# Performance work log

Measured on AMD Instinct MI355X. Metric: run time of the kernel, lower is better.

The kernel has to match this reference:

```python
import jax, jax.numpy as jnp
import numpy as np

N_NODES = 100000
N_EDGES = 1600000
IN_CH = 128
TYPE_EMB = 32
OUT_CH = 128
N_REL = 8
N_BASES = 8
N_NTYPES = 8
FEAT = IN_CH + TYPE_EMB  # 160, RGCNConv input dim after concat


def setup_inputs() -> dict:
    key = jax.random.key(0)
    ks = jax.random.split(key, 9)
    x = jax.random.normal(ks[0], (N_NODES, IN_CH), dtype=jnp.float32)
    node_type_ids = jax.random.randint(ks[1], (N_NODES,), 0, N_NTYPES)
    edge_index = jax.random.randint(ks[2], (2, N_EDGES), 0, N_NODES)
    edge_type = jax.random.randint(ks[3], (N_EDGES,), 0, N_REL)
    emb_table = jax.random.normal(ks[4], (N_NTYPES, TYPE_EMB), dtype=jnp.float32)
    bases = jax.random.normal(ks[5], (N_BASES, FEAT, OUT_CH), dtype=jnp.float32) * (1.0 / np.sqrt(FEAT))
    comp = jax.random.normal(ks[6], (N_REL, N_BASES), dtype=jnp.float32) * (1.0 / np.sqrt(N_BASES))
    root_w = jax.random.normal(ks[7], (FEAT, OUT_CH), dtype=jnp.float32) * (1.0 / np.sqrt(FEAT))
    bias = jnp.zeros((OUT_CH,), dtype=jnp.float32)
    return {"x": x, "node_type_ids": node_type_ids, "edge_index": edge_index,
            "edge_type": edge_type, "emb_table": emb_table, "bases": bases,
            "comp": comp, "root_w": root_w, "bias": bias}


def reference(x, node_type_ids, edge_index, edge_type, emb_table, bases, comp, root_w, bias):
    N = x.shape[0]
    # node-type embedding lookup + concat
    h = jnp.concatenate([x, emb_table[node_type_ids]], axis=1)  # [N, FEAT]
    # basis decomposition: per-relation weights [R, FEAT, OUT]
    weight = jnp.einsum('rb,bio->rio', comp, bases)
    src, dst = edge_index[0], edge_index[1]
    h_src = h[src]  # [E, FEAT] -- dominant gather
    # root/self transform + bias
    out = h @ root_w + bias
    # PyG RGCNConv default aggr='mean': per-relation mean over incoming edges, summed across relations
    for r in range(weight.shape[0]):
        m = (edge_type == r).astype(h.dtype)  # [E]
        s = jax.ops.segment_sum(h_src * m[:, None], dst, num_segments=N)  # [N, FEAT]
        c = jax.ops.segment_sum(m, dst, num_segments=N)                    # [N]
        mean_r = s / jnp.maximum(c, 1.0)[:, None]
        out = out + mean_r @ weight[r]
    # dropout is identity in eval mode
    return jax.nn.relu(out)
```

## Files before the change

### kernel.cpp

```cpp
#include <hip/hip_runtime.h>

#define NN 100000
#define NE 1600000
#define INC 128
#define TE 32
#define OC 128
#define NR 8
#define NBASES 8
#define FT 160
#define KP 168
#define KW 160
#define TN 64
#define NBKT 1563
#define NCH 512
#define EPB 3125
#define CAP 1536

typedef float f32x4 __attribute__((ext_vector_type(4)));
typedef __bf16 bf16x8 __attribute__((ext_vector_type(8)));

__device__ __forceinline__ unsigned f2bf1(float f) {
    unsigned u = __float_as_uint(f);
    return (u + 0x7fffu + ((u >> 16) & 1u)) >> 16;
}

__device__ __forceinline__ int bscan_excl(int v, int* tmp) {
    int tid = threadIdx.x;
    tmp[tid] = v; __syncthreads();
#pragma unroll
    for (int d = 1; d < 256; d <<= 1) {
        int t = (tid >= d) ? tmp[tid - d] : 0;
        __syncthreads();
        tmp[tid] += t;
        __syncthreads();
    }
    return tmp[tid] - v;
}

__global__ void k_prep(const float* __restrict__ x, const int* __restrict__ nt,
                       const float* __restrict__ emb, const float* __restrict__ comp,
                       const float* __restrict__ bases, const float* __restrict__ rootw,
                       unsigned short* __restrict__ h, unsigned short* __restrict__ Wt) {
    int idx = blockIdx.x * 256 + threadIdx.x;
    if (idx < 9 * 128 * KW) {
        int ridx = idx / (128 * KW);
        int rem  = idx % (128 * KW);
        int o = rem / KW;
        int k = rem % KW;
        float v;
        if (ridx < NR) {
            v = 0.f;
#pragma unroll
            for (int b = 0; b < NBASES; b++)
                v += comp[ridx * NBASES + b] * bases[(b * FT + k) * OC + o];
        } else {
            v = rootw[k * OC + o];
        }
        Wt[idx] = (unsigned short)f2bf1(v);
    }
    if (idx < NN * 20) {
        int n = idx / 20, c = idx % 20;
        f32x4 v0, v1;
        if (c < 16) {
            const float* p = x + (size_t)n * INC + c * 8;
            v0 = *(const f32x4*)p; v1 = *(const f32x4*)(p + 4);
        } else {
            int tt = nt[n];
            const float* p = emb + tt * TE + (c - 16) * 8;
            v0 = *(const f32x4*)p; v1 = *(const f32x4*)(p + 4);
        }
        uint4 o;
        o.x = f2bf1(v0.x) | (f2bf1(v0.y) << 16);
        o.y = f2bf1(v0.z) | (f2bf1(v0.w) << 16);
        o.z = f2bf1(v1.x) | (f2bf1(v1.y) << 16);
        o.w = f2bf1(v1.z) | (f2bf1(v1.w) << 16);
        *(uint4*)(h + (size_t)n * FT + c * 8) = o;
    }
}

__global__ __launch_bounds__(256) void k_hist(const int* __restrict__ ei, int* __restrict__ ghist) {
    __shared__ int hist[NBKT];
    int tid = threadIdx.x;
    for (int j = tid; j < NBKT; j += 256) hist[j] = 0;
    __syncthreads();
    int e0 = blockIdx.x * EPB;
#pragma unroll
    for (int k = 0; k < 13; k++) {
        int i = k * 256 + tid;
        if (i < EPB) atomicAdd(&hist[ei[NE + e0 + i] >> 6], 1);
    }
    __syncthreads();
    int* g = ghist + (size_t)blockIdx.x * NBKT;
    for (int j = tid; j < NBKT; j += 256) g[j] = hist[j];
}

__global__ void k_total(const int* __restrict__ ghist, int* __restrict__ total) {
    int j = blockIdx.x * 256 + threadIdx.x;
    if (j >= NBKT) return;
    int s = 0;
#pragma unroll 8
    for (int b = 0; b < NCH; b++) s += ghist[(size_t)b * NBKT + j];
    total[j] = s;
}

__global__ void k_scanTot(const int* __restrict__ total, int* __restrict__ bstart) {
    __shared__ int tmp[256];
    int tid = threadIdx.x, s = 0, i0 = tid * 7;
#pragma unroll
    for (int i = 0; i < 7; i++) { int j = i0 + i; if (j < NBKT) s += total[j]; }
    int run = bscan_excl(s, tmp);
#pragma unroll
    for (int i = 0; i < 7; i++) { int j = i0 + i; if (j < NBKT) { bstart[j] = run; run += total[j]; } }
    if (tid == 0) bstart[NBKT] = NE;
}

__global__ void k_offsets(int* __restrict__ ghist, const int* __restrict__ bstart) {
    int j = blockIdx.x * 256 + threadIdx.x;
    if (j >= NBKT) return;
    int run = bstart[j];
#pragma unroll 4
    for (int b = 0; b < NCH; b++) {
        int v = ghist[(size_t)b * NBKT + j];
        ghist[(size_t)b * NBKT + j] = run;
        run += v;
    }
}

__global__ __launch_bounds__(256) void k_scatter(const int* __restrict__ ei, const int* __restrict__ et,
                                                 const int* __restrict__ ghist, unsigned* __restrict__ slots) {
    __shared__ int cur[NBKT];
    int tid = threadIdx.x, b = blockIdx.x;
    for (int j = tid; j < NBKT; j += 256) cur[j] = ghist[(size_t)b * NBKT + j];
    __syncthreads();
    int e0 = b * EPB;
#pragma unroll
    for (int k = 0; k < 13; k++) {
        int i = k * 256 + tid;
        if (i < EPB) {
            int e = e0 + i;
            int s = ei[e], d = ei[NE + e], r = et[e];
            int pos = atomicAdd(&cur[d >> 6], 1);
            slots[pos] = (unsigned)s | ((unsigned)r << 17) | ((unsigned)(d & 63) << 20);
        }
    }
}

__global__ __launch_bounds__(256, 5) void k_mega(
    const unsigned short* __restrict__ h, const float* __restrict__ bias,
    const unsigned short* __restrict__ Wt, const int* __restrict__ bstart,
    const unsigned* __restrict__ slots, float* __restrict__ out) {
    __shared__ unsigned short featmem[TN * KP];
    __shared__ unsigned sl[CAP];
    __shared__ unsigned pkl[512];

    const int tid = threadIdx.x;
    const int lane = tid & 63;
    const int wave = tid >> 6;
    const int j = blockIdx.x;
    const int n0 = j * TN;

    unsigned* sl_in = reinterpret_cast<unsigned*>(featmem);
    int* hist = reinterpret_cast<int*>(featmem) + CAP;
    int* tmp  = reinterpret_cast<int*>(featmem) + CAP + 512;

    int s0 = bstart[j];
    int m = bstart[j + 1] - s0; if (m > CAP) m = CAP;
    for (int i = tid; i < m; i += 256) sl_in[i] = slots[s0 + i];
    for (int k = tid; k < 512; k += 256) hist[k] = 0;
    __syncthreads();
    for (int i = tid; i < m; i += 256) {
        unsigned v = sl_in[i];
        atomicAdd(&hist[((v >> 17) & 7u) * 64u + ((v >> 20) & 63u)], 1);
    }
    __syncthreads();
    int v0 = hist[2 * tid], v1 = hist[2 * tid + 1];
    int ex = bscan_excl(v0 + v1, tmp);
    pkl[2 * tid]     = (unsigned)ex | ((unsigned)v0 << 16);
    pkl[2 * tid + 1] = (unsigned)(ex + v0) | ((unsigned)v1 << 16);
    hist[2 * tid] = ex; hist[2 * tid + 1] = ex + v0;
    __syncthreads();
    for (int i = tid; i < m; i += 256) {
        unsigned v = sl_in[i];
        int p = atomicAdd(&hist[((v >> 17) & 7u) * 64u + ((v >> 20) & 63u)], 1);
        sl[p] = v & 0x03F1FFFFu;
    }
    __syncthreads();

    for (int i = tid; i < TN * 20; i += 256) {
        int nl = i / 20, c = i % 20, n = n0 + nl;
        uint4 v = (uint4){0u, 0u, 0u, 0u};
        if (n < NN) v = *reinterpret_cast<const uint4*>(h + (size_t)n * FT + c * 8);
        *reinterpret_cast<uint4*>(&featmem[nl * KP + c * 8]) = v;
    }

    f32x4 acc[8];
#pragma unroll
    for (int t = 0; t < 8; t++) acc[t] = (f32x4){0.f, 0.f, 0.f, 0.f};

    auto mfma_pass = [&](int ridx) {
        const unsigned short* fA = featmem + (lane & 15) * KP + ((lane >> 4) * 8);
        const unsigned short* gB = Wt + (size_t)ridx * 128 * KW
                                   + (wave * 32 + (lane & 15)) * KW + ((lane >> 4) * 8);
#pragma unroll
        for (int kc = 0; kc < 5; kc++) {
            bf16x8 a0 = *reinterpret_cast<const bf16x8*>(fA + 0 * 16 * KP + kc * 32);
            bf16x8 a1 = *reinterpret_cast<const bf16x8*>(fA + 1 * 16 * KP + kc * 32);
            bf16x8 a2 = *reinterpret_cast<const bf16x8*>(fA + 2 * 16 * KP + kc * 32);
            bf16x8 a3 = *reinterpret_cast<const bf16x8*>(fA + 3 * 16 * KP + kc * 32);
#pragma unroll
            for (int ct = 0; ct < 2; ct++) {
                bf16x8 b = *reinterpret_cast<const bf16x8*>(gB + ct * 16 * KW + kc * 32);
                acc[0 * 2 + ct] = __builtin_amdgcn_mfma_f32_16x16x32_bf16(a0, b, acc[0 * 2 + ct], 0, 0, 0);
                acc[1 * 2 + ct] = __builtin_amdgcn_mfma_f32_16x16x32_bf16(a1, b, acc[1 * 2 + ct], 0, 0, 0);
                acc[2 * 2 + ct] = __builtin_amdgcn_mfma_f32_16x16x32_bf16(a2, b, acc[2 * 2 + ct], 0, 0, 0);
                acc[3 * 2 + ct] = __builtin_amdgcn_mfma_f32_16x16x32_bf16(a3, b, acc[3 * 2 + ct], 0, 0, 0);
            }
        }
    };

    __syncthreads();
    mfma_pass(8);

    const int g = tid >> 4, l = tid & 15;
    const unsigned* hw = reinterpret_cast<const unsigned*>(h);
    for (int r = 0; r < NR; r++) {
        __syncthreads();
        int b0 = r * 64 + 4 * g;
        unsigned pa = pkl[b0], pd = pkl[b0 + 3];
        int sbeg = (int)(pa & 0xffffu);
        int send = (int)(pd & 0xffffu) + (int)(pd >> 16);
        float sa[10];
#pragma unroll
        for (int i = 0; i < 10; i++) sa[i] = 0.f;
        float run = 0.f;
        unsigned cur5[5]; int curdl = 0;
        if (sbeg < send) {
            unsigned v = sl[sbeg];
            const unsigned* hp = hw + (size_t)(v & 0x1FFFFu) * 80 + l;
#pragma unroll
            for (int c = 0; c < 5; c++) cur5[c] = hp[c * 16];
            curdl = (int)((v >> 20) & 63u);
        }
        for (int e = sbeg; e < send; e++) {
            int en = (e + 1 < send) ? e + 1 : e;
            unsigned vn = sl[en];
            const unsigned* hp = hw + (size_t)(vn & 0x1FFFFu) * 80 + l;
            unsigned nx[5];
#pragma unroll
            for (int c = 0; c < 5; c++) nx[c] = hp[c * 16];
            int nxdl = (int)((vn >> 20) & 63u);
#pragma unroll
            for (int c = 0; c < 5; c++) {
                sa[2 * c]     += __uint_as_float(cur5[c] << 16);
                sa[2 * c + 1] += __uint_as_float(cur5[c] & 0xFFFF0000u);
            }
            run += 1.f;
            bool fl = (e + 1 >= send) || (nxdl != curdl);
            if (fl) {
                float inv = 1.0f / run;
                unsigned* fp = reinterpret_cast<unsigned*>(featmem + curdl * KP) + l;
#pragma unroll
                for (int c = 0; c < 5; c++)
                    fp[c * 16] = f2bf1(sa[2 * c] * inv) | (f2bf1(sa[2 * c + 1] * inv) << 16);
#pragma unroll
                for (int i = 0; i < 10; i++) sa[i] = 0.f;
                run = 0.f;
            }
#pragma unroll
            for (int c = 0; c < 5; c++) cur5[c] = nx[c];
            curdl = nxdl;
        }
#pragma unroll
        for (int q = 0; q < 4; q++) {
            if ((pkl[b0 + q] >> 16) == 0u) {
                unsigned* fp = reinterpret_cast<unsigned*>(featmem + (4 * g + q) * KP) + l;
#pragma unroll
                for (int c = 0; c < 5; c++) fp[c * 16] = 0u;
            }
        }
        __syncthreads();
        mfma_pass(r);
    }

    const int rq = lane >> 4;
#pragma unroll
    for (int ct = 0; ct < 2; ct++) {
        int col = wave * 32 + ct * 16 + (lane & 15);
        float bv = bias[col];
#pragma unroll
        for (int rt = 0; rt < 4; rt++) {
#pragma unroll
            for (int i = 0; i < 4; i++) {
                int n = n0 + rt * 16 + rq * 4 + i;
                if (n < NN) {
                    float v = acc[rt * 2 + ct][i] + bv;
                    out[(size_t)n * OC + col] = v > 0.f ? v : 0.f;
                }
            }
        }
    }
}

extern "C" void kernel_launch(void* const* d_in, const int* in_sizes, int n_in,
                              void* d_out, int out_size, void* d_ws, size_t ws_size,
                              hipStream_t stream) {
    const float* x     = (const float*)d_in[0];
    const int*   ntype = (const int*)d_in[1];
    const int*   ei    = (const int*)d_in[2];
    const int*   et    = (const int*)d_in[3];
    const float* emb   = (const float*)d_in[4];
    const float* bases = (const float*)d_in[5];
    const float* comp  = (const float*)d_in[6];
    const float* rootw = (const float*)d_in[7];
    const float* bias  = (const float*)d_in[8];
    float* out = (float*)d_out;

    char* ws = (char*)d_ws;
    unsigned short* Wt     = (unsigned short*)(ws);
    unsigned short* h      = (unsigned short*)(ws + 368640);
    int*            ghist  = (int*)(ws + 32368640);
    int*            total  = (int*)(ws + 35569664);
    int*            bstart = (int*)(ws + 35576064);
    unsigned*       slots  = (unsigned*)(ws + 35582464);

    k_prep   <<<7813, 256, 0, stream>>>(x, ntype, emb, comp, bases, rootw, h, Wt);
    k_hist   <<<NCH,  256, 0, stream>>>(ei, ghist);
    k_total  <<<7,    256, 0, stream>>>(ghist, total);
    k_scanTot<<<1,    256, 0, stream>>>(total, bstart);
    k_offsets<<<7,    256, 0, stream>>>(ghist, bstart);
    k_scatter<<<NCH,  256, 0, stream>>>(ei, et, ghist, slots);
    k_mega   <<<NBKT, 256, 0, stream>>>(h, bias, Wt, bstart, slots, out);
}
```

Baseline: 372.4 us.

## Fuse histogram into prep kernel, coarsen edge chunks, unroll gather loop

Folds the edge histogram into the prep kernel as extra blocks, which removes one launch. The edge chunk count drops from 512 to 128, shrinking the per-chunk histogram arrays and the offset scan work that loops over chunks. The mega kernel's gather loop now issues four edges' row loads at once instead of one-ahead software pipelining, and its occupancy hint is relaxed from 5 to 4 blocks. Trade-offs: fewer, longer histogram and scatter blocks lower parallelism, and the unrolled gather raises register pressure.

Measured after the change: 353.2 us. -5.2%, faster.

```diff
diff --git a/kernel.cpp b/kernel.cpp
--- a/kernel.cpp
+++ b/kernel.cpp
@@ -12,8 +12,8 @@
 #define KW 160
 #define TN 64
 #define NBKT 1563
-#define NCH 512
-#define EPB 3125
+#define NCH 128
+#define EPB 12500
 #define CAP 1536
 
 typedef float f32x4 __attribute__((ext_vector_type(4)));
@@ -37,11 +37,31 @@
     return tmp[tid] - v;
 }
 
-__global__ void k_prep(const float* __restrict__ x, const int* __restrict__ nt,
-                       const float* __restrict__ emb, const float* __restrict__ comp,
-                       const float* __restrict__ bases, const float* __restrict__ rootw,
-                       unsigned short* __restrict__ h, unsigned short* __restrict__ Wt) {
-    int idx = blockIdx.x * 256 + threadIdx.x;
+__global__ __launch_bounds__(256) void k_prep(
+    const float* __restrict__ x, const int* __restrict__ nt,
+    const float* __restrict__ emb, const float* __restrict__ comp,
+    const float* __restrict__ bases, const float* __restrict__ rootw,
+    const int* __restrict__ ei,
+    unsigned short* __restrict__ h, unsigned short* __restrict__ Wt,
+    int* __restrict__ ghist) {
+    __shared__ int hist[NBKT];
+    int tid = threadIdx.x;
+    int b = blockIdx.x;
+    if (b < NCH) {
+        for (int j = tid; j < NBKT; j += 256) hist[j] = 0;
+        __syncthreads();
+        int e0 = b * EPB;
+#pragma unroll
+        for (int k = 0; k < 49; k++) {
+            int i = k * 256 + tid;
+            if (i < EPB) atomicAdd(&hist[ei[NE + e0 + i] >> 6], 1);
+        }
+        __syncthreads();
+        int* g = ghist + (size_t)b * NBKT;
+        for (int j = tid; j < NBKT; j += 256) g[j] = hist[j];
+        return;
+    }
+    int idx = (b - NCH) * 256 + tid;
     if (idx < 9 * 128 * KW) {
         int ridx = idx / (128 * KW);
         int rem  = idx % (128 * KW);
@@ -51,8 +71,8 @@
         if (ridx < NR) {
             v = 0.f;
 #pragma unroll
-            for (int b = 0; b < NBASES; b++)
-                v += comp[ridx * NBASES + b] * bases[(b * FT + k) * OC + o];
+            for (int bb = 0; bb < NBASES; bb++)
+                v += comp[ridx * NBASES + bb] * bases[(bb * FT + k) * OC + o];
         } else {
             v = rootw[k * OC + o];
         }
@@ -78,22 +98,6 @@
     }
 }
 
-__global__ __launch_bounds__(256) void k_hist(const int* __restrict__ ei, int* __restrict__ ghist) {
-    __shared__ int hist[NBKT];
-    int tid = threadIdx.x;
-    for (int j = tid; j < NBKT; j += 256) hist[j] = 0;
-    __syncthreads();
-    int e0 = blockIdx.x * EPB;
-#pragma unroll
-    for (int k = 0; k < 13; k++) {
-        int i = k * 256 + tid;
-        if (i < EPB) atomicAdd(&hist[ei[NE + e0 + i] >> 6], 1);
-    }
-    __syncthreads();
-    int* g = ghist + (size_t)blockIdx.x * NBKT;
-    for (int j = tid; j < NBKT; j += 256) g[j] = hist[j];
-}
-
 __global__ void k_total(const int* __restrict__ ghist, int* __restrict__ total) {
     int j = blockIdx.x * 256 + threadIdx.x;
     if (j >= NBKT) return;
@@ -134,7 +138,7 @@
     __syncthreads();
     int e0 = b * EPB;
 #pragma unroll
-    for (int k = 0; k < 13; k++) {
+    for (int k = 0; k < 49; k++) {
         int i = k * 256 + tid;
         if (i < EPB) {
             int e = e0 + i;
@@ -145,7 +149,7 @@
     }
 }
 
-__global__ __launch_bounds__(256, 5) void k_mega(
+__global__ __launch_bounds__(256, 4) void k_mega(
     const unsigned short* __restrict__ h, const float* __restrict__ bias,
     const unsigned short* __restrict__ Wt, const int* __restrict__ bstart,
     const unsigned* __restrict__ slots, float* __restrict__ out) {
@@ -233,42 +237,41 @@
 #pragma unroll
         for (int i = 0; i < 10; i++) sa[i] = 0.f;
         float run = 0.f;
-        unsigned cur5[5]; int curdl = 0;
-        if (sbeg < send) {
-            unsigned v = sl[sbeg];
-            const unsigned* hp = hw + (size_t)(v & 0x1FFFFu) * 80 + l;
-#pragma unroll
-            for (int c = 0; c < 5; c++) cur5[c] = hp[c * 16];
-            curdl = (int)((v >> 20) & 63u);
-        }
-        for (int e = sbeg; e < send; e++) {
-            int en = (e + 1 < send) ? e + 1 : e;
-            unsigned vn = sl[en];
-            const unsigned* hp = hw + (size_t)(vn & 0x1FFFFu) * 80 + l;
-            unsigned nx[5];
-#pragma unroll
-            for (int c = 0; c < 5; c++) nx[c] = hp[c * 16];
-            int nxdl = (int)((vn >> 20) & 63u);
-#pragma unroll
-            for (int c = 0; c < 5; c++) {
-                sa[2 * c]     += __uint_as_float(cur5[c] << 16);
-                sa[2 * c + 1] += __uint_as_float(cur5[c] & 0xFFFF0000u);
-            }
-            run += 1.f;
-            bool fl = (e + 1 >= send) || (nxdl != curdl);
-            if (fl) {
-                float inv = 1.0f / run;
-                unsigned* fp = reinterpret_cast<unsigned*>(featmem + curdl * KP) + l;
-#pragma unroll
-                for (int c = 0; c < 5; c++)
-                    fp[c * 16] = f2bf1(sa[2 * c] * inv) | (f2bf1(sa[2 * c + 1] * inv) << 16);
-#pragma unroll
-                for (int i = 0; i < 10; i++) sa[i] = 0.f;
-                run = 0.f;
-            }
-#pragma unroll
-            for (int c = 0; c < 5; c++) cur5[c] = nx[c];
-            curdl = nxdl;
+        for (int e = sbeg; e < send; e += 4) {
+            unsigned w[4][5];
+            int dl[4];
+#pragma unroll
+            for (int u = 0; u < 4; u++) {
+                int eu = e + u; if (eu >= send) eu = send - 1;
+                unsigned v = sl[eu];
+                const unsigned* hp = hw + (size_t)(v & 0x1FFFFu) * 80 + l;
+#pragma unroll
+                for (int c = 0; c < 5; c++) w[u][c] = hp[c * 16];
+                dl[u] = (int)((v >> 20) & 63u);
+            }
+#pragma unroll
+            for (int u = 0; u < 4; u++) {
+                if (e + u < send) {
+#pragma unroll
+                    for (int c = 0; c < 5; c++) {
+                        sa[2 * c]     += __uint_as_float(w[u][c] << 16);
+                        sa[2 * c + 1] += __uint_as_float(w[u][c] & 0xFFFF0000u);
+                    }
+                    run += 1.f;
+                    bool last = (e + u + 1 >= send);
+                    int ndl = last ? -1 : (int)((sl[e + u + 1] >> 20) & 63u);
+                    if (last || ndl != dl[u]) {
+                        float inv = 1.0f / run;
+                        unsigned* fp = reinterpret_cast<unsigned*>(featmem + dl[u] * KP) + l;
+#pragma unroll
+                        for (int c = 0; c < 5; c++)
+                            fp[c * 16] = f2bf1(sa[2 * c] * inv) | (f2bf1(sa[2 * c + 1] * inv) << 16);
+#pragma unroll
+                        for (int i = 0; i < 10; i++) sa[i] = 0.f;
+                        run = 0.f;
+                    }
+                }
+            }
         }
 #pragma unroll
         for (int q = 0; q < 4; q++) {
@@ -319,12 +322,11 @@
     unsigned short* Wt     = (unsigned short*)(ws);
     unsigned short* h      = (unsigned short*)(ws + 368640);
     int*            ghist  = (int*)(ws + 32368640);
-    int*            total  = (int*)(ws + 35569664);
-    int*            bstart = (int*)(ws + 35576064);
-    unsigned*       slots  = (unsigned*)(ws + 35582464);
-
-    k_prep   <<<7813, 256, 0, stream>>>(x, ntype, emb, comp, bases, rootw, h, Wt);
-    k_hist   <<<NCH,  256, 0, stream>>>(ei, ghist);
+    int*            total  = (int*)(ws + 33168896);
+    int*            bstart = (int*)(ws + 33175296);
+    unsigned*       slots  = (unsigned*)(ws + 33181696);
+
+    k_prep   <<<NCH + 7813, 256, 0, stream>>>(x, ntype, emb, comp, bases, rootw, ei, h, Wt, ghist);
     k_total  <<<7,    256, 0, stream>>>(ghist, total);
     k_scanTot<<<1,    256, 0, stream>>>(total, bstart);
     k_offsets<<<7,    256, 0, stream>>>(ghist, bstart);
```
